# Kernel optimization log

Measured on AMD Instinct MI355X. Metric: run time of the kernel, lower is better.

Reference implementation:

```python
import jax, jax.numpy as jnp
import numpy as np

B, D_IN, D_HID, D_OUT = 16384, 512, 512, 512
E, K = 8, 2
VQ_COEFF, LB_COEFF = 0.05, 0.01
LOG100 = float(np.log(100.0))
LOG2 = float(np.log(2.0))


def _normalize(v):
    # torch F.normalize(dim=1): x / max(||x||, 1e-12)
    n = jnp.linalg.norm(v, axis=-1, keepdims=True)
    return v / jnp.maximum(n, 1e-12)


def _cv_squared(v):
    # torch .var() is unbiased (ddof=1)
    return jnp.var(v, ddof=1) / (jnp.mean(v) ** 2 + 1e-10)


def _rbm_layer(x, rm, W, b, ca, temp):
    # x: [B, d_in], rm: [E, d_in], W: [E, d_out, d_in], b: [E, d_out]
    rm_n = jax.lax.stop_gradient(_normalize(rm))          # .detach() in source
    nx = _normalize(x)
    dists = nx @ rm_n.T                                    # [B, E]
    top_v, top_i = jax.lax.top_k(dists, K)                 # [B, K]
    tv = jax.nn.softmax(top_v, axis=-1)                    # softmax over top-k
    bsz = dists.shape[0]
    attn = jnp.zeros_like(dists).at[jnp.arange(bsz)[:, None], top_i].set(tv)
    # const_attention is frozen (requires_grad=False)
    inp_att = jnp.exp(jnp.minimum(jax.lax.stop_gradient(ca), LOG100))  # [E]
    # dense gather-compute-scatter: expert e output for every token, masked by attn
    eo = jnp.einsum('bi,eoi->beo', x, W) * inp_att[None, :, None] + b[None, :, :]
    out = jnp.einsum('be,beo->bo', jax.lax.stop_gradient(attn), eo)    # att.detach()
    out = out * jnp.exp(jnp.minimum(temp, LOG100))
    # aux losses (eval mode: no EMA memory update)
    vq = -(nx[:, None, :] * rm_n[top_i]).sum(-1)           # [B, K]
    vq_loss = (tv * vq).sum(-1).mean()
    lb = _cv_squared(attn.sum(0))
    aux = VQ_COEFF * vq_loss + LB_COEFF * lb               # sim_coeff = 0
    return out, aux


def setup_inputs() -> dict:
    key = jax.random.key(0)
    ks = jax.random.split(key, 8)
    x = jax.random.normal(ks[0], (B, D_IN), dtype=jnp.float32)
    rm0 = _normalize(jax.random.normal(ks[1], (E, D_IN), dtype=jnp.float32))
    W0 = jax.random.normal(ks[2], (E, D_HID, D_IN), dtype=jnp.float32) / np.sqrt(D_IN)
    b0 = jnp.zeros((E, D_HID), dtype=jnp.float32)
    rm1 = _normalize(jax.random.normal(ks[3], (E, D_HID), dtype=jnp.float32))
    W1 = jax.random.normal(ks[4], (E, D_OUT, D_HID), dtype=jnp.float32) / np.sqrt(D_HID)
    b1 = jnp.zeros((E, D_OUT), dtype=jnp.float32)
    temp0 = jnp.full((1,), LOG2, dtype=jnp.float32)
    temp1 = jnp.full((1,), LOG2, dtype=jnp.float32)
    ca0 = jnp.zeros((E,), dtype=jnp.float32)
    ca1 = jnp.zeros((E,), dtype=jnp.float32)
    return {"x": x, "rm0": rm0, "W0": W0, "b0": b0, "temp0": temp0, "ca0": ca0,
            "rm1": rm1, "W1": W1, "b1": b1, "temp1": temp1, "ca1": ca1}


def reference(x, rm0, W0, b0, temp0, ca0, rm1, W1, b1, temp1, ca1):
    h0, a0 = _rbm_layer(x, rm0, W0, b0, ca0, temp0)
    h_emb = h0                      # embedding tapped after layer 0 (pre-activation)
    h = jax.nn.relu(h0)             # norm_type=None -> no norm
    h1, a1 = _rbm_layer(h, rm1, W1, b1, ca1, temp1)
    return (h_emb, h1, a0 + a1)
```

## Files before the change

### kernel.cpp

```cpp
#include <hip/hip_runtime.h>
#include <cmath>
#include <cstdint>

#define NTOK   16384
#define NEXP   8
#define DM     512
#define LOG100 4.605170185988092f

typedef _Float16 half8  __attribute__((ext_vector_type(8)));
typedef float    floatx4 __attribute__((ext_vector_type(4)));

#define MFMA_F16(a, b, c) __builtin_amdgcn_mfma_f32_16x16x32_f16((a), (b), (c), 0, 0, 0)

__device__ __forceinline__ void gl_lds16(const void* g, void* l) {
    __builtin_amdgcn_global_load_lds(
        (const __attribute__((address_space(1))) void*)g,
        (__attribute__((address_space(3))) void*)l, 16, 0, 0);
}


__global__ __launch_bounds__(256) void prep_kernel(
    const float* __restrict__ rm0, const float* __restrict__ rm1,
    const float* __restrict__ ca0, const float* __restrict__ ca1,
    const float* __restrict__ temp0, const float* __restrict__ temp1,
    float* __restrict__ ctrl, float* __restrict__ rmn)
{
    int tid = threadIdx.x, lane = tid & 63, w = tid >> 6;
    if (tid < 32) ((int*)ctrl)[tid] = 0;
    if (tid >= 32 && tid < 48) ctrl[tid] = 0.f;
    if (tid == 48 || tid == 49) ctrl[tid] = 0.f;
    if (tid == 50) ctrl[50] = expf(fminf(temp0[0], LOG100));
    if (tid == 51) ctrl[51] = expf(fminf(temp1[0], LOG100));
    if (tid >= 52 && tid < 68) {
        int i = tid - 52;
        ctrl[tid] = expf(fminf(i < 8 ? ca0[i] : ca1[i - 8], LOG100));
    }
    for (int r = w; r < 16; r += 4) {
        const float* src = (r < 8) ? (rm0 + r * DM) : (rm1 + (r - 8) * DM);
        float v[8]; float ss = 0.f;
        #pragma unroll
        for (int j = 0; j < 8; ++j) { v[j] = src[lane + 64 * j]; ss += v[j] * v[j]; }
        #pragma unroll
        for (int off = 32; off > 0; off >>= 1) ss += __shfl_xor(ss, off);
        float inv = 1.f / fmaxf(sqrtf(ss), 1e-12f);
        float* dst = rmn + r * DM;
        #pragma unroll
        for (int j = 0; j < 8; ++j) dst[lane + 64 * j] = v[j] * inv;
    }
}

__global__ __launch_bounds__(256) void pack_w_kernel(
    const float* __restrict__ W0, const float* __restrict__ W1,
    half8* __restrict__ w0pk, half8* __restrict__ w1pk)
{
    int i = blockIdx.x * 256 + threadIdx.x;
    if (i < 512 * 1024) {
        int l = i & 63, j = (i >> 6) & 15, kb = (i >> 10) & 15, nt = (i >> 14) & 3, e = i >> 16;
        int s = l >> 3, p = l & 7, c = p ^ s;
        int n = nt * 128 + j * 8 + s;
        int k = kb * 32 + (c & 3) * 8;
        const float* src = W0 + ((size_t)e * DM + n) * DM + k;
        half8 v;
        #pragma unroll
        for (int t = 0; t < 8; ++t) {
            float f = src[t];
            _Float16 h = (_Float16)f;
            v[t] = (c < 4) ? h : (_Float16)(f - (float)h);
        }
        w0pk[i] = v;
    } else {
        int m = i - 512 * 1024;
        int l = m & 63, j = (m >> 6) & 15, kb = (m >> 10) & 7, nt = (m >> 13) & 3, e = m >> 15;
        int s = l >> 3, p = l & 7, c = p ^ s;
        int n = nt * 128 + j * 8 + s;
        int k = kb * 64 + c * 8;
        const float* src = W1 + ((size_t)e * DM + n) * DM + k;
        half8 v;
        #pragma unroll
        for (int t = 0; t < 8; ++t) v[t] = (_Float16)src[t];
        w1pk[m] = v;
    }
}

__global__ __launch_bounds__(256) void route_kernel(
    const float* __restrict__ src,
    const float* __restrict__ rmn,
    int relu_in, int split,
    _Float16* __restrict__ dst,
    unsigned char* __restrict__ key,
    float2* __restrict__ wts,
    float2* __restrict__ bs)
{
    __shared__ float rmLds[NEXP * DM];
    int tid = threadIdx.x;
    for (int i = tid; i < NEXP * DM; i += 256) rmLds[i] = rmn[i];
    __syncthreads();
    int lane = tid & 63, w = tid >> 6;
    int token = blockIdx.x * 4 + w;

    const float* row = src + (size_t)token * DM;
    float x[8]; float ss = 0.f;
    #pragma unroll
    for (int j = 0; j < 8; ++j) {
        float v = row[lane + 64 * j];
        if (relu_in) v = fmaxf(v, 0.f);
        x[j] = v; ss += v * v;
    }
    if (split) {
        #pragma unroll
        for (int j = 0; j < 8; ++j) {
            int k = lane + 64 * j;
            size_t base = (size_t)token * 1024 + (size_t)((k >> 5) << 6) + (k & 31);
            _Float16 h = (_Float16)x[j];
            dst[base] = h;
            dst[base + 32] = (_Float16)(x[j] - (float)h);
        }
    } else {
        #pragma unroll
        for (int j = 0; j < 8; ++j)
            dst[(size_t)token * DM + lane + 64 * j] = (_Float16)x[j];
    }
    float d[8];
    #pragma unroll
    for (int e = 0; e < 8; ++e) {
        float a = 0.f;
        #pragma unroll
        for (int j = 0; j < 8; ++j) a += x[j] * rmLds[e * DM + lane + 64 * j];
        d[e] = a;
    }
    #pragma unroll
    for (int off = 32; off > 0; off >>= 1) {
        ss += __shfl_xor(ss, off);
        #pragma unroll
        for (int e = 0; e < 8; ++e) d[e] += __shfl_xor(d[e], off);
    }
    float inv = 1.f / fmaxf(sqrtf(ss), 1e-12f);
    float best = -1e30f, second = -1e30f; int be = 0, se = 0;
    #pragma unroll
    for (int e = 0; e < 8; ++e) {
        float de = d[e] * inv;
        if (de > best)        { second = best; se = be; best = de; be = e; }
        else if (de > second) { second = de; se = e; }
    }
    float z = expf(second - best);
    float w0 = 1.f / (1.f + z), w1 = z / (1.f + z);
    if (lane == 0) {
        key[token] = (unsigned char)be;
        key[NTOK + token] = (unsigned char)se;
        wts[token] = make_float2(w0, w1);
        bs[token] = make_float2(best, second);
    }
}

__global__ __launch_bounds__(256) void compact_kernel(
    const unsigned char* __restrict__ key,
    const float2* __restrict__ wts,
    const float2* __restrict__ bs,
    int* __restrict__ cnt,
    unsigned short* __restrict__ bkt,
    float* __restrict__ imp,
    float* __restrict__ vq_acc)
{
    int slot = blockIdx.x >> 3, e = blockIdx.x & 7;
    int chunk = blockIdx.y;
    const unsigned char* k = key + slot * NTOK;
    unsigned short* ob = bkt + (size_t)(slot * 8 + e) * NTOK;
    int tid = threadIdx.x, lane = tid & 63, w = tid >> 6;
    float wsum = 0.f, vqs = 0.f;
    for (int c = 0; c < 8; ++c) {
        int tok = chunk * 2048 + c * 256 + tid;
        bool m = (k[tok] == (unsigned char)e);
        unsigned long long mask = __ballot(m);
        int wcount = __popcll(mask);
        int wbase = 0;
        if (lane == 0 && wcount) wbase = atomicAdd(&cnt[slot * 8 + e], wcount);
        wbase = __shfl(wbase, 0);
        if (m) {
            int pre = __popcll(mask & ((1ull << lane) - 1ull));
            ob[wbase + pre] = (unsigned short)tok;
            float2 wp = wts[tok]; float2 b2 = bs[tok];
            float wv = slot ? wp.y : wp.x;
            wsum += wv;
            vqs  += wv * (slot ? b2.y : b2.x);
        }
    }
    #pragma unroll
    for (int off = 32; off > 0; off >>= 1) {
        wsum += __shfl_xor(wsum, off);
        vqs  += __shfl_xor(vqs, off);
    }
    __shared__ float rw[4], rv[4];
    if (lane == 0) { rw[w] = wsum; rv[w] = vqs; }
    __syncthreads();
    if (tid == 0) {
        atomicAdd(&imp[e], rw[0] + rw[1] + rw[2] + rw[3]);
        atomicAdd(vq_acc, -(rv[0] + rv[1] + rv[2] + rv[3]));
    }
}

template <bool SPLIT>
__global__ __launch_bounds__(256) void gemm_kernel(
    const _Float16* __restrict__ A,
    const _Float16* __restrict__ Wpk,
    const float* __restrict__ bias,
    const float* __restrict__ iav,
    const float* __restrict__ tscp,
    const int* __restrict__ cnt,
    const unsigned short* __restrict__ bkt,
    const float2* __restrict__ wts,
    int slot, int accum,
    float* __restrict__ outp)
{
    __shared__ __align__(16) _Float16 lds[2 * 16384];
    __shared__ int tokLds[128];

    int p = blockIdx.x;
    int xcd = p & 7, s = p >> 3;
    int t = xcd * 17 + (s >> 2), nt = s & 3;
    int e = -1, m0 = 0, M = 0, acc = 0;
    #pragma unroll
    for (int ee = 0; ee < 8; ++ee) {
        int Me = cnt[ee];
        int ne = (Me + 127) >> 7;
        if (t >= acc && t < acc + ne) { e = ee; m0 = (t - acc) << 7; M = Me; }
        acc += ne;
    }
    if (e < 0) return;
    int n0 = nt << 7;
    int valid = min(128, M - m0);
    int tid = threadIdx.x, lane = tid & 63, w = tid >> 6;
    if (tid < 128) tokLds[tid] = bkt[e * NTOK + m0 + min(tid, valid - 1)];
    __syncthreads();

    int subRow = lane >> 3, pp = lane & 7;
    int cSt = pp ^ subRow;
    int wm = w >> 1, wn = w & 1;
    int r0 = wm * 64, c0 = wn * 64;
    int q = lane >> 4, l15 = lane & 15;

    constexpr int KIT = SPLIT ? 16 : 8;
    constexpr int AS  = SPLIT ? 1024 : 512;

    int tokR[4];
    #pragma unroll
    for (int jj = 0; jj < 4; ++jj) tokR[jj] = tokLds[(w + jj * 4) * 8 + subRow];

    const _Float16* wtile = Wpk + (size_t)(e * 4 + nt) * KIT * 8192;

    floatx4 accu[4][4];
    #pragma unroll
    for (int mi = 0; mi < 4; ++mi)
        #pragma unroll
        for (int ni = 0; ni < 4; ++ni) accu[mi][ni] = (floatx4){0.f, 0.f, 0.f, 0.f};

    auto stage = [&](int kb, int buf) {
        _Float16* dA = lds + buf * 16384;
        _Float16* dB = dA + 8192;
        #pragma unroll
        for (int jj = 0; jj < 4; ++jj) {
            int j = w + jj * 4;
            gl_lds16(A + (size_t)tokR[jj] * AS + kb * 64 + cSt * 8, (void*)(dA + j * 512));
        }
        const _Float16* wb = wtile + (size_t)kb * 8192;
        #pragma unroll
        for (int jj = 0; jj < 4; ++jj) {
            int j = w + jj * 4;
            gl_lds16(wb + j * 512 + lane * 8, (void*)(dB + j * 512));
        }
    };

    auto compute = [&](int buf) {
        const _Float16* bA = lds + buf * 16384;
        const _Float16* bB = bA + 8192;
        if constexpr (SPLIT) {
            half8 ah[4], al[4];
            #pragma unroll
            for (int mi = 0; mi < 4; ++mi) {
                int r = r0 + mi * 16 + l15;
                int ph = q ^ (r & 7), pl = (q + 4) ^ (r & 7);
                ah[mi] = *(const half8*)(bA + r * 64 + ph * 8);
                al[mi] = *(const half8*)(bA + r * 64 + pl * 8);
            }
            #pragma unroll
            for (int ni = 0; ni < 4; ++ni) {
                int r = c0 + ni * 16 + l15;
                int ph = q ^ (r & 7), pl = (q + 4) ^ (r & 7);
                half8 bh = *(const half8*)(bB + r * 64 + ph * 8);
                half8 bl = *(const half8*)(bB + r * 64 + pl * 8);
                #pragma unroll
                for (int mi = 0; mi < 4; ++mi) accu[mi][ni] = MFMA_F16(ah[mi], bh, accu[mi][ni]);
                #pragma unroll
                for (int mi = 0; mi < 4; ++mi) accu[mi][ni] = MFMA_F16(ah[mi], bl, accu[mi][ni]);
                #pragma unroll
                for (int mi = 0; mi < 4; ++mi) accu[mi][ni] = MFMA_F16(al[mi], bh, accu[mi][ni]);
            }
        } else {
            #pragma unroll
            for (int ks = 0; ks < 2; ++ks) {
                half8 a[4];
                #pragma unroll
                for (int mi = 0; mi < 4; ++mi) {
                    int r = r0 + mi * 16 + l15;
                    int pc = (ks * 4 + q) ^ (r & 7);
                    a[mi] = *(const half8*)(bA + r * 64 + pc * 8);
                }
                #pragma unroll
                for (int ni = 0; ni < 4; ++ni) {
                    int r = c0 + ni * 16 + l15;
                    int pc = (ks * 4 + q) ^ (r & 7);
                    half8 b = *(const half8*)(bB + r * 64 + pc * 8);
                    #pragma unroll
                    for (int mi = 0; mi < 4; ++mi) accu[mi][ni] = MFMA_F16(a[mi], b, accu[mi][ni]);
                }
            }
        }
    };

    stage(0, 0);
    stage(1, 1);
    for (int kb = 0; kb < KIT - 1; ++kb) {
        asm volatile("s_waitcnt vmcnt(8)" ::: "memory");
        __builtin_amdgcn_s_barrier();
        __builtin_amdgcn_sched_barrier(0);
        compute(kb & 1);
        __builtin_amdgcn_sched_barrier(0);
        __builtin_amdgcn_s_barrier();
        if (kb + 2 < KIT) stage(kb + 2, kb & 1);
    }
    asm volatile("s_waitcnt vmcnt(0)" ::: "memory");
    __builtin_amdgcn_s_barrier();
    __builtin_amdgcn_sched_barrier(0);
    compute((KIT - 1) & 1);

    float tsc = *tscp, iae = iav[e];
    float bv[4];
    #pragma unroll
    for (int ni = 0; ni < 4; ++ni) bv[ni] = bias[e * DM + n0 + c0 + ni * 16 + l15];
    #pragma unroll
    for (int mi = 0; mi < 4; ++mi) {
        int liBase = r0 + mi * 16 + q * 4;
        #pragma unroll
        for (int reg = 0; reg < 4; ++reg) {
            int li = liBase + reg;
            if (li < valid) {
                int tok = tokLds[li];
                float2 wp = wts[tok];
                float wgt = slot ? wp.y : wp.x;
                float sg = tsc * wgt * iae, sb = tsc * wgt;
                float* orow = outp + (size_t)tok * DM + n0;
                #pragma unroll
                for (int ni = 0; ni < 4; ++ni) {
                    float v = accu[mi][ni][reg] * sg + bv[ni] * sb;
                    int c = c0 + ni * 16 + l15;
                    if (accum) orow[c] += v; else orow[c] = v;
                }
            }
        }
    }
}

__global__ void finalize_kernel(const float* __restrict__ ctrl, float* __restrict__ outp)
{
    if (threadIdx.x == 0) {
        float aux = 0.f;
        for (int l = 0; l < 2; ++l) {
            float vq = ctrl[48 + l] / (float)NTOK;
            float mean = 0.f;
            for (int e = 0; e < 8; ++e) mean += ctrl[32 + l * 8 + e];
            mean *= 0.125f;
            float s = 0.f;
            for (int e = 0; e < 8; ++e) {
                float d = ctrl[32 + l * 8 + e] - mean;
                s += d * d;
            }
            float var = s / 7.f;
            float lb = var / (mean * mean + 1e-10f);
            aux += 0.05f * vq + 0.01f * lb;
        }
        *outp = aux;
    }
}

extern "C" void kernel_launch(void* const* d_in, const int* in_sizes, int n_in,
                              void* d_out, int out_size, void* d_ws, size_t ws_size,
                              hipStream_t stream) {
    const float* x     = (const float*)d_in[0];
    const float* rm0   = (const float*)d_in[1];
    const float* W0    = (const float*)d_in[2];
    const float* b0    = (const float*)d_in[3];
    const float* temp0 = (const float*)d_in[4];
    const float* ca0   = (const float*)d_in[5];
    const float* rm1   = (const float*)d_in[6];
    const float* W1    = (const float*)d_in[7];
    const float* b1    = (const float*)d_in[8];
    const float* temp1 = (const float*)d_in[9];
    const float* ca1   = (const float*)d_in[10];
    float* out = (float*)d_out;

    char* ws = (char*)d_ws;
    float* ctrl = (float*)ws;
    int*   cnt  = (int*)ctrl;
    float* imp  = ctrl + 32;
    float* vq   = ctrl + 48;
    float* tsc  = ctrl + 50;
    float* ia   = ctrl + 52;
    float* rmn  = ctrl + 128;
    float2*        wts = (float2*)(ws + (size_t)64  * 1024);
    float2*        bs  = (float2*)(ws + (size_t)384 * 1024);
    unsigned char* key = (unsigned char*)(ws + (size_t)704 * 1024);

    char* big = ws + (1 << 20);
    half8*          w0pk8 = (half8*)(big);
    half8*          w1pk8 = (half8*)(big + (size_t)8  * 1024 * 1024);
    const _Float16* w0pk  = (const _Float16*)w0pk8;
    const _Float16* w1pk  = (const _Float16*)w1pk8;
    _Float16*       h16   = (_Float16*)(big + (size_t)12 * 1024 * 1024);
    unsigned short* bkt   = (unsigned short*)(big + (size_t)28 * 1024 * 1024);

    _Float16* xpk = (_Float16*)(out + (size_t)NTOK * DM);

    prep_kernel<<<1, 256, 0, stream>>>(rm0, rm1, ca0, ca1, temp0, temp1, ctrl, rmn);
    pack_w_kernel<<<3072, 256, 0, stream>>>(W0, W1, w0pk8, w1pk8);

    route_kernel<<<4096, 256, 0, stream>>>(x, rmn, 0, 1, xpk, key, wts, bs);
    compact_kernel<<<dim3(16, 8), 256, 0, stream>>>(key, wts, bs, cnt, bkt, imp, vq);
    gemm_kernel<true><<<544, 256, 0, stream>>>(xpk, w0pk, b0, ia, tsc,
        cnt, bkt, wts, 0, 0, out);
    gemm_kernel<true><<<544, 256, 0, stream>>>(xpk, w0pk, b0, ia, tsc,
        cnt + 8, bkt + 8 * NTOK, wts, 1, 1, out);

    route_kernel<<<4096, 256, 0, stream>>>(out, rmn + 4096, 1, 0, h16,
        key + 2 * NTOK, wts + NTOK, bs + NTOK);
    compact_kernel<<<dim3(16, 8), 256, 0, stream>>>(key + 2 * NTOK, wts + NTOK, bs + NTOK,
        cnt + 16, bkt + 16 * NTOK, imp + 8, vq + 1);
    gemm_kernel<false><<<544, 256, 0, stream>>>(h16, w1pk, b1, ia + 8, tsc + 1,
        cnt + 16, bkt + 16 * NTOK, wts + NTOK, 0, 0, out + (size_t)NTOK * DM);
    gemm_kernel<false><<<544, 256, 0, stream>>>(h16, w1pk, b1, ia + 8, tsc + 1,
        cnt + 24, bkt + 24 * NTOK, wts + NTOK, 1, 1, out + (size_t)NTOK * DM);

    finalize_kernel<<<1, 64, 0, stream>>>(ctrl, out + (size_t)2 * NTOK * DM);
}
```

Before: 464.9 us.

## Load gathered A rows directly to registers, stage only weights through LDS

The grouped expert GEMM no longer stages the gathered token rows (A) through LDS. Each lane now loads its MFMA A fragments straight from global memory, while only the weight tile is double-buffered in LDS. This halves the LDS footprint, allowing a launch_bounds occupancy hint of 3 blocks per CU, and removes A-side LDS writes and reads. The cost is uncoalesced 16-byte global gathers per lane that sit on the critical path, with less latency hiding than the old two-stage prefetch, plus single-stage weight prefetch and more register pressure.

New measurement: 485.3 us. 1.04x slower.

```diff
diff --git a/kernel.cpp b/kernel.cpp
--- a/kernel.cpp
+++ b/kernel.cpp
@@ -199,7 +199,7 @@
 }
 
 template <bool SPLIT>
-__global__ __launch_bounds__(256) void gemm_kernel(
+__global__ __launch_bounds__(256, 3) void gemm_kernel(
     const _Float16* __restrict__ A,
     const _Float16* __restrict__ Wpk,
     const float* __restrict__ bias,
@@ -211,19 +211,19 @@
     int slot, int accum,
     float* __restrict__ outp)
 {
-    __shared__ __align__(16) _Float16 lds[2 * 16384];
+    __shared__ __align__(16) _Float16 ldsB[2 * 8192];
     __shared__ int tokLds[128];
 
     int p = blockIdx.x;
     int xcd = p & 7, s = p >> 3;
     int t = xcd * 17 + (s >> 2), nt = s & 3;
-    int e = -1, m0 = 0, M = 0, acc = 0;
+    int e = -1, m0 = 0, M = 0, acc0 = 0;
     #pragma unroll
     for (int ee = 0; ee < 8; ++ee) {
         int Me = cnt[ee];
         int ne = (Me + 127) >> 7;
-        if (t >= acc && t < acc + ne) { e = ee; m0 = (t - acc) << 7; M = Me; }
-        acc += ne;
+        if (t >= acc0 && t < acc0 + ne) { e = ee; m0 = (t - acc0) << 7; M = Me; }
+        acc0 += ne;
     }
     if (e < 0) return;
     int n0 = nt << 7;
@@ -232,8 +232,6 @@
     if (tid < 128) tokLds[tid] = bkt[e * NTOK + m0 + min(tid, valid - 1)];
     __syncthreads();
 
-    int subRow = lane >> 3, pp = lane & 7;
-    int cSt = pp ^ subRow;
     int wm = w >> 1, wn = w & 1;
     int r0 = wm * 64, c0 = wn * 64;
     int q = lane >> 4, l15 = lane & 15;
@@ -241,9 +239,10 @@
     constexpr int KIT = SPLIT ? 16 : 8;
     constexpr int AS  = SPLIT ? 1024 : 512;
 
-    int tokR[4];
-    #pragma unroll
-    for (int jj = 0; jj < 4; ++jj) tokR[jj] = tokLds[(w + jj * 4) * 8 + subRow];
+    const _Float16* Ab[4];
+    #pragma unroll
+    for (int mi = 0; mi < 4; ++mi)
+        Ab[mi] = A + (size_t)tokLds[r0 + mi * 16 + l15] * AS + q * 8;
 
     const _Float16* wtile = Wpk + (size_t)(e * 4 + nt) * KIT * 8192;
 
@@ -253,84 +252,61 @@
         #pragma unroll
         for (int ni = 0; ni < 4; ++ni) accu[mi][ni] = (floatx4){0.f, 0.f, 0.f, 0.f};
 
-    auto stage = [&](int kb, int buf) {
-        _Float16* dA = lds + buf * 16384;
-        _Float16* dB = dA + 8192;
-        #pragma unroll
-        for (int jj = 0; jj < 4; ++jj) {
-            int j = w + jj * 4;
-            gl_lds16(A + (size_t)tokR[jj] * AS + kb * 64 + cSt * 8, (void*)(dA + j * 512));
-        }
-        const _Float16* wb = wtile + (size_t)kb * 8192;
-        #pragma unroll
-        for (int jj = 0; jj < 4; ++jj) {
-            int j = w + jj * 4;
-            gl_lds16(wb + j * 512 + lane * 8, (void*)(dB + j * 512));
-        }
-    };
-
-    auto compute = [&](int buf) {
-        const _Float16* bA = lds + buf * 16384;
-        const _Float16* bB = bA + 8192;
-        if constexpr (SPLIT) {
-            half8 ah[4], al[4];
+    #pragma unroll
+    for (int jj = 0; jj < 4; ++jj) {
+        int j = w + jj * 4;
+        gl_lds16(wtile + j * 512 + lane * 8, (void*)(ldsB + j * 512));
+    }
+
+    #pragma unroll
+    for (int kb = 0; kb < KIT; ++kb) {
+        half8 ah[4], al[4];
+        #pragma unroll
+        for (int mi = 0; mi < 4; ++mi) {
+            ah[mi] = *(const half8*)(Ab[mi] + kb * 64);
+            al[mi] = *(const half8*)(Ab[mi] + kb * 64 + 32);
+        }
+        if (kb + 1 < KIT) {
+            _Float16* dB = ldsB + ((kb + 1) & 1) * 8192;
+            const _Float16* wb = wtile + (size_t)(kb + 1) * 8192;
             #pragma unroll
-            for (int mi = 0; mi < 4; ++mi) {
-                int r = r0 + mi * 16 + l15;
-                int ph = q ^ (r & 7), pl = (q + 4) ^ (r & 7);
-                ah[mi] = *(const half8*)(bA + r * 64 + ph * 8);
-                al[mi] = *(const half8*)(bA + r * 64 + pl * 8);
+            for (int jj = 0; jj < 4; ++jj) {
+                int j = w + jj * 4;
+                gl_lds16(wb + j * 512 + lane * 8, (void*)(dB + j * 512));
             }
+        }
+        if (kb + 1 < KIT) asm volatile("s_waitcnt vmcnt(12)" ::: "memory");
+        else              asm volatile("s_waitcnt vmcnt(8)"  ::: "memory");
+        __builtin_amdgcn_sched_barrier(0);
+        __builtin_amdgcn_s_barrier();
+        {
+            const _Float16* bB = ldsB + (kb & 1) * 8192;
             #pragma unroll
             for (int ni = 0; ni < 4; ++ni) {
                 int r = c0 + ni * 16 + l15;
                 int ph = q ^ (r & 7), pl = (q + 4) ^ (r & 7);
                 half8 bh = *(const half8*)(bB + r * 64 + ph * 8);
                 half8 bl = *(const half8*)(bB + r * 64 + pl * 8);
-                #pragma unroll
-                for (int mi = 0; mi < 4; ++mi) accu[mi][ni] = MFMA_F16(ah[mi], bh, accu[mi][ni]);
-                #pragma unroll
-                for (int mi = 0; mi < 4; ++mi) accu[mi][ni] = MFMA_F16(ah[mi], bl, accu[mi][ni]);
-                #pragma unroll
-                for (int mi = 0; mi < 4; ++mi) accu[mi][ni] = MFMA_F16(al[mi], bh, accu[mi][ni]);
-            }
-        } else {
-            #pragma unroll
-            for (int ks = 0; ks < 2; ++ks) {
-                half8 a[4];
-                #pragma unroll
-                for (int mi = 0; mi < 4; ++mi) {
-                    int r = r0 + mi * 16 + l15;
-                    int pc = (ks * 4 + q) ^ (r & 7);
-                    a[mi] = *(const half8*)(bA + r * 64 + pc * 8);
-                }
-                #pragma unroll
-                for (int ni = 0; ni < 4; ++ni) {
-                    int r = c0 + ni * 16 + l15;
-                    int pc = (ks * 4 + q) ^ (r & 7);
-                    half8 b = *(const half8*)(bB + r * 64 + pc * 8);
+                if constexpr (SPLIT) {
                     #pragma unroll
-                    for (int mi = 0; mi < 4; ++mi) accu[mi][ni] = MFMA_F16(a[mi], b, accu[mi][ni]);
+                    for (int mi = 0; mi < 4; ++mi) accu[mi][ni] = MFMA_F16(ah[mi], bh, accu[mi][ni]);
+                    #pragma unroll
+                    for (int mi = 0; mi < 4; ++mi) accu[mi][ni] = MFMA_F16(ah[mi], bl, accu[mi][ni]);
+                    #pragma unroll
+                    for (int mi = 0; mi < 4; ++mi) accu[mi][ni] = MFMA_F16(al[mi], bh, accu[mi][ni]);
+                } else {
+                    #pragma unroll
+                    for (int mi = 0; mi < 4; ++mi) accu[mi][ni] = MFMA_F16(ah[mi], bh, accu[mi][ni]);
+                    #pragma unroll
+                    for (int mi = 0; mi < 4; ++mi) accu[mi][ni] = MFMA_F16(al[mi], bl, accu[mi][ni]);
                 }
             }
         }
-    };
-
-    stage(0, 0);
-    stage(1, 1);
-    for (int kb = 0; kb < KIT - 1; ++kb) {
-        asm volatile("s_waitcnt vmcnt(8)" ::: "memory");
-        __builtin_amdgcn_s_barrier();
-        __builtin_amdgcn_sched_barrier(0);
-        compute(kb & 1);
-        __builtin_amdgcn_sched_barrier(0);
-        __builtin_amdgcn_s_barrier();
-        if (kb + 2 < KIT) stage(kb + 2, kb & 1);
-    }
-    asm volatile("s_waitcnt vmcnt(0)" ::: "memory");
-    __builtin_amdgcn_s_barrier();
-    __builtin_amdgcn_sched_barrier(0);
-    compute((KIT - 1) & 1);
+        if (kb + 1 < KIT) {
+            __builtin_amdgcn_sched_barrier(0);
+            __builtin_amdgcn_s_barrier();
+        }
+    }
 
     float tsc = *tscp, iae = iav[e];
     float bv[4];
```
